# Performance work log

Measured on AMD Instinct MI355X. Metric: run time of the kernel, lower is better.

## Reference

```python
import jax, jax.numpy as jnp
import numpy as np

IN_FEATURES = 4096
OUT_FEATURES = 4096
NNZ = 838860
BATCH = 512


def setup_inputs() -> dict:
    key = jax.random.key(0)
    kx, kr, kc, kv, kb = jax.random.split(key, 5)
    x = jax.random.normal(kx, (BATCH, IN_FEATURES), dtype=jnp.float32)
    row_idx = jax.random.randint(kr, (NNZ,), 0, OUT_FEATURES, dtype=jnp.int64)
    col_idx = jax.random.randint(kc, (NNZ,), 0, IN_FEATURES, dtype=jnp.int64)
    values = jax.random.normal(kv, (NNZ,), dtype=jnp.float32)
    bias = jax.random.normal(kb, (OUT_FEATURES,), dtype=jnp.float32)
    return {"x": x, "row_idx": row_idx, "col_idx": col_idx,
            "values": values, "bias": bias}


def reference(x, row_idx, col_idx, values, bias):
    # COO sparse linear: y[b, row] += x[b, col] * val, then add bias.
    x_flat = x.reshape(-1, IN_FEATURES)                    # [B, in]
    weighted = x_flat[:, col_idx] * values                 # [B, nnz]
    out = jnp.zeros((x_flat.shape[0], OUT_FEATURES), dtype=x.dtype)
    out = out.at[:, row_idx].add(weighted)                 # scatter-add per row
    out = out + bias
    return out.reshape(x.shape[:-1] + (OUT_FEATURES,))
```

## Files before the change

### kernel.cpp

```cpp
#include <hip/hip_runtime.h>

#define IN_F    4096
#define OUT_F   4096
#define K_DIM   4096
#define NNZ_C   838860
#define BATCH   512
#define BK      32
#define BM      128
#define BN      128

typedef short bf16x8 __attribute__((ext_vector_type(8)));
typedef float f32x4  __attribute__((ext_vector_type(4)));

__device__ __forceinline__ unsigned short f2bf(float f) {
    unsigned u = __float_as_uint(f);
    u += 0x7fffu + ((u >> 16) & 1u);
    return (unsigned short)(u >> 16);
}
__device__ __forceinline__ void gload_lds16(const void* g, void* l) {
    __builtin_amdgcn_global_load_lds(
        (const __attribute__((address_space(1))) unsigned int*)g,
        (__attribute__((address_space(3))) unsigned int*)l, 16, 0, 0);
}

#define N_WZ   (OUT_F * K_DIM / 8)
#define N_CVT  (BATCH * K_DIM / 8)
#define N_OUT  (BATCH * OUT_F / 4)
__global__ void prep(const float* __restrict__ x,
                     unsigned short* __restrict__ xb,
                     const float* __restrict__ bias,
                     float* __restrict__ out,
                     uint4* __restrict__ Wz, int do_bias) {
    int i = blockIdx.x * 256 + threadIdx.x;
    if (i < N_WZ) { Wz[i] = make_uint4(0, 0, 0, 0); return; }
    i -= N_WZ;
    if (i < N_CVT) {
        const float4* p = (const float4*)x + (size_t)i * 2;
        float4 a = p[0], b = p[1];
        union { unsigned short h[8]; bf16x8 v; } u;
        u.h[0] = f2bf(a.x); u.h[1] = f2bf(a.y); u.h[2] = f2bf(a.z); u.h[3] = f2bf(a.w);
        u.h[4] = f2bf(b.x); u.h[5] = f2bf(b.y); u.h[6] = f2bf(b.z); u.h[7] = f2bf(b.w);
        ((bf16x8*)xb)[i] = u.v;
        return;
    }
    i -= N_CVT;
    if (i < N_OUT && do_bias) {
        float4 b = ((const float4*)bias)[i & (OUT_F / 4 - 1)];
        ((float4*)out)[i] = b;
    }
}
#define PREP_BLOCKS ((N_WZ + N_CVT + N_OUT) / 256)

__global__ void scatter_pk(const int* __restrict__ row_idx,
                           const int* __restrict__ col_idx,
                           const float* __restrict__ values,
                           unsigned short* __restrict__ W) {
    int i = blockIdx.x * 256 + threadIdx.x;
    if (i >= NNZ_C / 4) return;
    int4   r4 = ((const int4*)row_idx)[i];
    int4   c4 = ((const int4*)col_idx)[i];
    float4 v4 = ((const float4*)values)[i];
#pragma unroll
    for (int j = 0; j < 4; ++j) {
        int r = (&r4.x)[j], c = (&c4.x)[j];
        float v = (&v4.x)[j];
        unsigned idx = (unsigned)r * K_DIM + (unsigned)c;
        unsigned short h = f2bf(v);
        unsigned data = (idx & 1u) ? ((unsigned)h << 16) : (unsigned)h;
        unsigned long long addr = (unsigned long long)(W + (idx & ~1u));
        asm volatile("global_atomic_pk_add_bf16 %0, %1, off"
                     :: "v"(addr), "v"(data) : "memory");
    }
}

template <int EPI, int SK>
__global__ void __launch_bounds__(256)
gemm_bt(const unsigned short* __restrict__ Abf,
        const unsigned short* __restrict__ Wbf,
        const float* __restrict__ bias,
        float* __restrict__ out,
        float* __restrict__ parts) {
    __shared__ __align__(16) unsigned short As[2][BM * BK];
    __shared__ __align__(16) unsigned short Bs[2][BN * BK];

    const int nt = blockIdx.x, mt = blockIdx.y, s = blockIdx.z;
    const int t = threadIdx.x, w = t >> 6, ln = t & 63;
    const int wm = w & 1, wn = w >> 1;
    const int KSs = K_DIM / SK;
    const int ks0 = s * KSs;

    const int srow = w * 16 + (ln >> 2);
    const int scol = (((ln & 3) ^ ((ln >> 3) & 3)) * 8);
    const unsigned short* gA0 = Abf + (size_t)(mt * BM + srow) * K_DIM + ks0 + scol;
    const unsigned short* gA1 = gA0 + (size_t)64 * K_DIM;
    const unsigned short* gB0 = Wbf + (size_t)(nt * BN + srow) * K_DIM + ks0 + scol;
    const unsigned short* gB1 = gB0 + (size_t)64 * K_DIM;
    const int lA0o = (w * 16) * BK;
    const int lA1o = (64 + w * 16) * BK;

    const int quad = ln >> 4, lanem = ln & 15;
    const int rsw = (quad ^ ((lanem >> 1) & 3)) * 8;
    const int rAo = (wm * 64 + lanem) * BK + rsw;
    const int rBo = (wn * 64 + lanem) * BK + rsw;

    f32x4 acc[4][4];
#pragma unroll
    for (int mi = 0; mi < 4; ++mi)
#pragma unroll
        for (int ni = 0; ni < 4; ++ni)
            acc[mi][ni] = (f32x4){0.f, 0.f, 0.f, 0.f};

    auto stage = [&](int p, int kt) {
        gload_lds16(gA0 + kt * BK, &As[p][lA0o]);
        gload_lds16(gA1 + kt * BK, &As[p][lA1o]);
        gload_lds16(gB0 + kt * BK, &Bs[p][lA0o]);
        gload_lds16(gB1 + kt * BK, &Bs[p][lA1o]);
    };

    const int NK = KSs / BK;
    stage(0, 0);
    __syncthreads();

#pragma unroll 2
    for (int kt = 0; kt < NK; ++kt) {
        const int p = kt & 1;
        if (kt + 1 < NK) stage(p ^ 1, kt + 1);

        const unsigned short* rA = &As[p][0] + rAo;
        const unsigned short* rB = &Bs[p][0] + rBo;
        bf16x8 af[4], bfr[4];
#pragma unroll
        for (int mi = 0; mi < 4; ++mi) af[mi]  = *(const bf16x8*)(rA + mi * 16 * BK);
#pragma unroll
        for (int ni = 0; ni < 4; ++ni) bfr[ni] = *(const bf16x8*)(rB + ni * 16 * BK);
#pragma unroll
        for (int mi = 0; mi < 4; ++mi)
#pragma unroll
            for (int ni = 0; ni < 4; ++ni)
                acc[mi][ni] = __builtin_amdgcn_mfma_f32_16x16x32_bf16(
                    af[mi], bfr[ni], acc[mi][ni], 0, 0, 0);

        __syncthreads();
    }

    const int row0 = mt * BM + wm * 64 + quad * 4;
    const int col0 = nt * BN + wn * 64 + lanem;
    if (EPI == 0) {
        float bv[4];
#pragma unroll
        for (int ni = 0; ni < 4; ++ni) bv[ni] = (s == 0) ? bias[col0 + ni * 16] : 0.f;
        float* dst = (s == 0) ? out : parts + (size_t)(s - 1) * BATCH * OUT_F;
#pragma unroll
        for (int mi = 0; mi < 4; ++mi)
#pragma unroll
            for (int ni = 0; ni < 4; ++ni)
#pragma unroll
                for (int r = 0; r < 4; ++r)
                    dst[(size_t)(row0 + mi * 16 + r) * OUT_F + col0 + ni * 16] =
                        acc[mi][ni][r] + bv[ni];
    } else {
#pragma unroll
        for (int mi = 0; mi < 4; ++mi)
#pragma unroll
            for (int ni = 0; ni < 4; ++ni)
#pragma unroll
                for (int r = 0; r < 4; ++r)
                    atomicAdd(&out[(size_t)(row0 + mi * 16 + r) * OUT_F + col0 + ni * 16],
                              acc[mi][ni][r]);
    }
}

__global__ void reduce_parts(float* __restrict__ out,
                             const float* __restrict__ parts) {
    int i = blockIdx.x * 256 + threadIdx.x;
    float4 a = ((const float4*)out)[i];
#pragma unroll
    for (int p = 0; p < 7; ++p) {
        float4 b = ((const float4*)(parts + (size_t)p * BATCH * OUT_F))[i];
        a.x += b.x; a.y += b.y; a.z += b.z; a.w += b.w;
    }
    ((float4*)out)[i] = a;
}

extern "C" void kernel_launch(void* const* d_in, const int* in_sizes, int n_in,
                              void* d_out, int out_size, void* d_ws, size_t ws_size,
                              hipStream_t stream) {
    const float* x       = (const float*)d_in[0];
    const int*   row_idx = (const int*)d_in[1];
    const int*   col_idx = (const int*)d_in[2];
    const float* values  = (const float*)d_in[3];
    const float* bias    = (const float*)d_in[4];
    float*       out     = (float*)d_out;

    unsigned short* xb = (unsigned short*)d_ws;
    unsigned short* W  = xb + (size_t)BATCH * K_DIM;
    float* parts = (float*)(W + (size_t)OUT_F * K_DIM);
    size_t need = (size_t)BATCH * K_DIM * 2 + (size_t)OUT_F * K_DIM * 2
                + (size_t)7 * BATCH * OUT_F * 4;
    bool use_parts = (ws_size >= need);

    prep<<<PREP_BLOCKS, 256, 0, stream>>>(x, xb, bias, out, (uint4*)W,
                                          use_parts ? 0 : 1);
    scatter_pk<<<(NNZ_C / 4 + 255) / 256, 256, 0, stream>>>(
        row_idx, col_idx, values, W);

    if (use_parts) {
        gemm_bt<0, 8><<<dim3(OUT_F / BN, BATCH / BM, 8), 256, 0, stream>>>(
            xb, W, bias, out, parts);
        reduce_parts<<<BATCH * OUT_F / 4 / 256, 256, 0, stream>>>(out, parts);
    } else {
        gemm_bt<1, 4><<<dim3(OUT_F / BN, BATCH / BM, 4), 256, 0, stream>>>(
            xb, W, bias, out, nullptr);
    }
}
```

Measured before the change: 163.8 us.

## Fuse split-K reduction into GEMM via last-block counter; merge scatter with convert

Each GEMM tile now increments a global per-tile counter, and the last split-K block sums the partial buffers into the output, which removes the separate reduce_parts kernel. The bf16 conversion of x and the bias init now run in the same kernel as the scatter atomics. The zero_w kernel resets the counters. In exchange the GEMM takes on fences and a serialized tail reduction done by only 128 blocks, which risks imbalance at the end of the launch.

```diff
diff --git a/kernel.cpp b/kernel.cpp
--- a/kernel.cpp
+++ b/kernel.cpp
@@ -23,53 +23,65 @@
         (__attribute__((address_space(3))) unsigned int*)l, 16, 0, 0);
 }
 
+__device__ int g_cnt[128];
+
 #define N_WZ   (OUT_F * K_DIM / 8)
-#define N_CVT  (BATCH * K_DIM / 8)
-#define N_OUT  (BATCH * OUT_F / 4)
-__global__ void prep(const float* __restrict__ x,
-                     unsigned short* __restrict__ xb,
-                     const float* __restrict__ bias,
-                     float* __restrict__ out,
-                     uint4* __restrict__ Wz, int do_bias) {
+__global__ void zero_w(uint4* __restrict__ Wz) {
+    if (blockIdx.x == 0 && threadIdx.x < 128) g_cnt[threadIdx.x] = 0;
     int i = blockIdx.x * 256 + threadIdx.x;
-    if (i < N_WZ) { Wz[i] = make_uint4(0, 0, 0, 0); return; }
-    i -= N_WZ;
-    if (i < N_CVT) {
+    Wz[i] = make_uint4(0, 0, 0, 0);
+}
+#define ZW_BLOCKS (N_WZ / 256)
+
+#define N_CVT   (BATCH * K_DIM / 8)
+#define N_OUT   (BATCH * OUT_F / 4)
+#define NS_BLK  ((NNZ_C / 4 + 255) / 256)
+#define NC_BLK  (N_CVT / 256)
+#define NB_BLK  (N_OUT / 256)
+__global__ void scatcvt(const int* __restrict__ row_idx,
+                        const int* __restrict__ col_idx,
+                        const float* __restrict__ values,
+                        unsigned short* __restrict__ W,
+                        const float* __restrict__ x,
+                        unsigned short* __restrict__ xb,
+                        const float* __restrict__ bias,
+                        float* __restrict__ out) {
+    int b = blockIdx.x;
+    if (b < NS_BLK) {
+        int i = b * 256 + threadIdx.x;
+        if (i >= NNZ_C / 4) return;
+        int4   r4 = ((const int4*)row_idx)[i];
+        int4   c4 = ((const int4*)col_idx)[i];
+        float4 v4 = ((const float4*)values)[i];
+#pragma unroll
+        for (int j = 0; j < 4; ++j) {
+            int r = (&r4.x)[j], c = (&c4.x)[j];
+            float v = (&v4.x)[j];
+            unsigned idx = (unsigned)r * K_DIM + (unsigned)c;
+            unsigned short h = f2bf(v);
+            unsigned data = (idx & 1u) ? ((unsigned)h << 16) : (unsigned)h;
+            unsigned long long addr = (unsigned long long)(W + (idx & ~1u));
+            asm volatile("global_atomic_pk_add_bf16 %0, %1, off"
+                         :: "v"(addr), "v"(data) : "memory");
+        }
+        return;
+    }
+    b -= NS_BLK;
+    if (b < NC_BLK) {
+        int i = b * 256 + threadIdx.x;
         const float4* p = (const float4*)x + (size_t)i * 2;
-        float4 a = p[0], b = p[1];
+        float4 a = p[0], bb = p[1];
         union { unsigned short h[8]; bf16x8 v; } u;
-        u.h[0] = f2bf(a.x); u.h[1] = f2bf(a.y); u.h[2] = f2bf(a.z); u.h[3] = f2bf(a.w);
-        u.h[4] = f2bf(b.x); u.h[5] = f2bf(b.y); u.h[6] = f2bf(b.z); u.h[7] = f2bf(b.w);
+        u.h[0] = f2bf(a.x);  u.h[1] = f2bf(a.y);  u.h[2] = f2bf(a.z);  u.h[3] = f2bf(a.w);
+        u.h[4] = f2bf(bb.x); u.h[5] = f2bf(bb.y); u.h[6] = f2bf(bb.z); u.h[7] = f2bf(bb.w);
         ((bf16x8*)xb)[i] = u.v;
         return;
     }
-    i -= N_CVT;
-    if (i < N_OUT && do_bias) {
-        float4 b = ((const float4*)bias)[i & (OUT_F / 4 - 1)];
-        ((float4*)out)[i] = b;
-    }
-}
-#define PREP_BLOCKS ((N_WZ + N_CVT + N_OUT) / 256)
-
-__global__ void scatter_pk(const int* __restrict__ row_idx,
-                           const int* __restrict__ col_idx,
-                           const float* __restrict__ values,
-                           unsigned short* __restrict__ W) {
-    int i = blockIdx.x * 256 + threadIdx.x;
-    if (i >= NNZ_C / 4) return;
-    int4   r4 = ((const int4*)row_idx)[i];
-    int4   c4 = ((const int4*)col_idx)[i];
-    float4 v4 = ((const float4*)values)[i];
-#pragma unroll
-    for (int j = 0; j < 4; ++j) {
-        int r = (&r4.x)[j], c = (&c4.x)[j];
-        float v = (&v4.x)[j];
-        unsigned idx = (unsigned)r * K_DIM + (unsigned)c;
-        unsigned short h = f2bf(v);
-        unsigned data = (idx & 1u) ? ((unsigned)h << 16) : (unsigned)h;
-        unsigned long long addr = (unsigned long long)(W + (idx & ~1u));
-        asm volatile("global_atomic_pk_add_bf16 %0, %1, off"
-                     :: "v"(addr), "v"(data) : "memory");
+    b -= NC_BLK;
+    int i = b * 256 + threadIdx.x;
+    if (i < N_OUT) {
+        float4 bb = ((const float4*)bias)[i & (OUT_F / 4 - 1)];
+        ((float4*)out)[i] = bb;
     }
 }
 
@@ -158,6 +170,31 @@
                 for (int r = 0; r < 4; ++r)
                     dst[(size_t)(row0 + mi * 16 + r) * OUT_F + col0 + ni * 16] =
                         acc[mi][ni][r] + bv[ni];
+
+        __threadfence();
+        __syncthreads();
+        __shared__ int lastflag;
+        if (t == 0)
+            lastflag = (atomicAdd(&g_cnt[mt * (OUT_F / BN) + nt], 1) == SK - 1);
+        __syncthreads();
+        if (!lastflag) return;
+        __threadfence();
+
+        const float4* o4r = (const float4*)out;
+        float4*       o4w = (float4*)out;
+        for (int i = t; i < BM * (BN / 4); i += 256) {
+            int rr = i >> 5, cc = i & 31;
+            size_t idx = (size_t)(mt * BM + rr) * (OUT_F / 4)
+                       + (size_t)nt * (BN / 4) + cc;
+            float4 a = o4r[idx];
+#pragma unroll
+            for (int pp = 0; pp < SK - 1; ++pp) {
+                float4 bq = ((const float4*)(parts
+                              + (size_t)pp * BATCH * OUT_F))[idx];
+                a.x += bq.x; a.y += bq.y; a.z += bq.z; a.w += bq.w;
+            }
+            o4w[idx] = a;
+        }
     } else {
 #pragma unroll
         for (int mi = 0; mi < 4; ++mi)
@@ -168,18 +205,6 @@
                     atomicAdd(&out[(size_t)(row0 + mi * 16 + r) * OUT_F + col0 + ni * 16],
                               acc[mi][ni][r]);
     }
-}
-
-__global__ void reduce_parts(float* __restrict__ out,
-                             const float* __restrict__ parts) {
-    int i = blockIdx.x * 256 + threadIdx.x;
-    float4 a = ((const float4*)out)[i];
-#pragma unroll
-    for (int p = 0; p < 7; ++p) {
-        float4 b = ((const float4*)(parts + (size_t)p * BATCH * OUT_F))[i];
-        a.x += b.x; a.y += b.y; a.z += b.z; a.w += b.w;
-    }
-    ((float4*)out)[i] = a;
 }
 
 extern "C" void kernel_launch(void* const* d_in, const int* in_sizes, int n_in,
@@ -199,15 +224,15 @@
                 + (size_t)7 * BATCH * OUT_F * 4;
     bool use_parts = (ws_size >= need);
 
-    prep<<<PREP_BLOCKS, 256, 0, stream>>>(x, xb, bias, out, (uint4*)W,
-                                          use_parts ? 0 : 1);
-    scatter_pk<<<(NNZ_C / 4 + 255) / 256, 256, 0, stream>>>(
-        row_idx, col_idx, values, W);
+    zero_w<<<ZW_BLOCKS, 256, 0, stream>>>((uint4*)W);
+
+    int sc_blocks = NS_BLK + NC_BLK + (use_parts ? 0 : NB_BLK);
+    scatcvt<<<sc_blocks, 256, 0, stream>>>(row_idx, col_idx, values, W,
+                                           x, xb, bias, out);
 
     if (use_parts) {
         gemm_bt<0, 8><<<dim3(OUT_F / BN, BATCH / BM, 8), 256, 0, stream>>>(
             xb, W, bias, out, parts);
-        reduce_parts<<<BATCH * OUT_F / 4 / 256, 256, 0, stream>>>(out, parts);
     } else {
         gemm_bt<1, 4><<<dim3(OUT_F / BN, BATCH / BM, 4), 256, 0, stream>>>(
             xb, W, bias, out, nullptr);
```

Result: slower. 315.6 us (+92.7%).

## Drop double buffering for single-stage BK=64 loop and one-nnz-per-thread scatter

Applied to the files above, without the earlier changes.

The GEMM main loop now fills both LDS buffers with consecutive K=32 slices, so each iteration covers K=64, with two barriers per iteration instead of one. Loads for the next step are issued only after compute finishes, so global-to-LDS transfer no longer overlaps MFMA work. This gives fewer iterations and fewer barriers per K element but exposes load latency within each workgroup. The scatter kernel also moves from four nonzeros per thread with vector loads to one nonzero per thread with scalar loads, which raises parallelism for the atomics.

```diff
diff --git a/kernel.cpp b/kernel.cpp
--- a/kernel.cpp
+++ b/kernel.cpp
@@ -56,21 +56,15 @@
                            const float* __restrict__ values,
                            unsigned short* __restrict__ W) {
     int i = blockIdx.x * 256 + threadIdx.x;
-    if (i >= NNZ_C / 4) return;
-    int4   r4 = ((const int4*)row_idx)[i];
-    int4   c4 = ((const int4*)col_idx)[i];
-    float4 v4 = ((const float4*)values)[i];
-#pragma unroll
-    for (int j = 0; j < 4; ++j) {
-        int r = (&r4.x)[j], c = (&c4.x)[j];
-        float v = (&v4.x)[j];
-        unsigned idx = (unsigned)r * K_DIM + (unsigned)c;
-        unsigned short h = f2bf(v);
-        unsigned data = (idx & 1u) ? ((unsigned)h << 16) : (unsigned)h;
-        unsigned long long addr = (unsigned long long)(W + (idx & ~1u));
-        asm volatile("global_atomic_pk_add_bf16 %0, %1, off"
-                     :: "v"(addr), "v"(data) : "memory");
-    }
+    if (i >= NNZ_C) return;
+    int r = row_idx[i], c = col_idx[i];
+    float v = values[i];
+    unsigned idx = (unsigned)r * K_DIM + (unsigned)c;
+    unsigned short h = f2bf(v);
+    unsigned data = (idx & 1u) ? ((unsigned)h << 16) : (unsigned)h;
+    unsigned long long addr = (unsigned long long)(W + (idx & ~1u));
+    asm volatile("global_atomic_pk_add_bf16 %0, %1, off"
+                 :: "v"(addr), "v"(data) : "memory");
 }
 
 template <int EPI, int SK>
@@ -110,37 +104,39 @@
         for (int ni = 0; ni < 4; ++ni)
             acc[mi][ni] = (f32x4){0.f, 0.f, 0.f, 0.f};
 
-    auto stage = [&](int p, int kt) {
-        gload_lds16(gA0 + kt * BK, &As[p][lA0o]);
-        gload_lds16(gA1 + kt * BK, &As[p][lA1o]);
-        gload_lds16(gB0 + kt * BK, &Bs[p][lA0o]);
-        gload_lds16(gB1 + kt * BK, &Bs[p][lA1o]);
+    auto stage = [&](int kt) {
+#pragma unroll
+        for (int ks = 0; ks < 2; ++ks) {
+            const int off = kt * 64 + ks * BK;
+            gload_lds16(gA0 + off, &As[ks][lA0o]);
+            gload_lds16(gA1 + off, &As[ks][lA1o]);
+            gload_lds16(gB0 + off, &Bs[ks][lA0o]);
+            gload_lds16(gB1 + off, &Bs[ks][lA1o]);
+        }
     };
 
-    const int NK = KSs / BK;
-    stage(0, 0);
-    __syncthreads();
-
-#pragma unroll 2
+    const int NK = KSs / 64;
+    stage(0);
     for (int kt = 0; kt < NK; ++kt) {
-        const int p = kt & 1;
-        if (kt + 1 < NK) stage(p ^ 1, kt + 1);
-
-        const unsigned short* rA = &As[p][0] + rAo;
-        const unsigned short* rB = &Bs[p][0] + rBo;
-        bf16x8 af[4], bfr[4];
-#pragma unroll
-        for (int mi = 0; mi < 4; ++mi) af[mi]  = *(const bf16x8*)(rA + mi * 16 * BK);
-#pragma unroll
-        for (int ni = 0; ni < 4; ++ni) bfr[ni] = *(const bf16x8*)(rB + ni * 16 * BK);
-#pragma unroll
-        for (int mi = 0; mi < 4; ++mi)
-#pragma unroll
-            for (int ni = 0; ni < 4; ++ni)
-                acc[mi][ni] = __builtin_amdgcn_mfma_f32_16x16x32_bf16(
-                    af[mi], bfr[ni], acc[mi][ni], 0, 0, 0);
-
         __syncthreads();
+#pragma unroll
+        for (int ks = 0; ks < 2; ++ks) {
+            const unsigned short* rA = &As[ks][0] + rAo;
+            const unsigned short* rB = &Bs[ks][0] + rBo;
+            bf16x8 af[4], bfr[4];
+#pragma unroll
+            for (int mi = 0; mi < 4; ++mi) af[mi]  = *(const bf16x8*)(rA + mi * 16 * BK);
+#pragma unroll
+            for (int ni = 0; ni < 4; ++ni) bfr[ni] = *(const bf16x8*)(rB + ni * 16 * BK);
+#pragma unroll
+            for (int mi = 0; mi < 4; ++mi)
+#pragma unroll
+                for (int ni = 0; ni < 4; ++ni)
+                    acc[mi][ni] = __builtin_amdgcn_mfma_f32_16x16x32_bf16(
+                        af[mi], bfr[ni], acc[mi][ni], 0, 0, 0);
+        }
+        __syncthreads();
+        if (kt + 1 < NK) stage(kt + 1);
     }
 
     const int row0 = mt * BM + wm * 64 + quad * 4;
@@ -201,7 +197,7 @@
 
     prep<<<PREP_BLOCKS, 256, 0, stream>>>(x, xb, bias, out, (uint4*)W,
                                           use_parts ? 0 : 1);
-    scatter_pk<<<(NNZ_C / 4 + 255) / 256, 256, 0, stream>>>(
+    scatter_pk<<<(NNZ_C + 255) / 256, 256, 0, stream>>>(
         row_idx, col_idx, values, W);
 
     if (use_parts) {
```

Result: faster. 158.2 us (-3.4%).
